# Performance work log

Measured on AMD Instinct MI355X. Metric: run time of the kernel, lower is better.

Reference implementation:

```python
import jax, jax.numpy as jnp
import numpy as np
from jax import lax

N = 200; E = 3200; HID = 64; NH = 16; OUT = 2 * HID; CAT = NH * OUT  # CAT = 2048
ALPHA = 0.2


def _gat(h, e_attr, adj, n2n, W, a_s, a_d, a_e, We, concat):
    # edge-feature-aware GAT head: logits from Wh_i, Wh_j and projected node2node feats
    Nn = h.shape[0]
    Wh = h @ W                                       # [N, out]
    ee = ((n2n @ We) @ a_e).reshape(Nn, Nn)          # [N, N] edge-feature term
    logits = jax.nn.leaky_relu((Wh @ a_s)[:, None] + (Wh @ a_d)[None, :] + ee,
                               negative_slope=ALPHA)
    logits = jnp.where(adj > 0, logits, -1e9)        # mask to graph structure
    att = jax.nn.softmax(logits, axis=1)
    h2 = att @ Wh
    if concat:
        h2 = jax.nn.elu(h2)
    return h2, jax.nn.elu(e_attr @ We)               # updated node + edge features


def _edge_pool(x, eidx, e, w, b):
    # static-shape edge pooling: score edges, gate nodes by mean incident score
    src, dst = eidx[0], eidx[1]
    s = jax.nn.sigmoid(jnp.concatenate([x[src], x[dst], e], axis=1) @ w + b)  # [E]
    deg = jax.ops.segment_sum(jnp.ones_like(s), src, num_segments=x.shape[0])
    ns = jax.ops.segment_sum(s, src, num_segments=x.shape[0]) / (deg + 1e-6)
    return x * ns[:, None], e * s[:, None]


def _gpool(x, w, b):
    # GlobalAttention: gate_nn = Linear+Sigmoid, softmax over nodes, weighted sum
    gate = jax.nn.softmax(jax.nn.sigmoid(x @ w + b), axis=0)  # [N, 1]
    return jnp.sum(gate * x, axis=0, keepdims=True)           # [1, D]


def _adj_n2n(Nn, eidx, eattr):
    # vectorized version of the per-edge Python loop in _get_adj_node2node
    src, dst = eidx[0], eidx[1]
    adj = jnp.zeros((Nn, Nn), eattr.dtype).at[src, dst].set(1.0)
    n2n = jnp.zeros((Nn * Nn, eattr.shape[1]), eattr.dtype).at[src * Nn + dst].set(eattr)
    return adj, n2n


def _lstm_dir(x, Wih, Whh, b):
    # one LSTM direction over seq x [T, Din] (PyTorch i,f,g,o gate order)
    Hh = Whh.shape[1]
    def step(carry, xt):
        h, c = carry
        g = xt @ Wih.T + h @ Whh.T + b
        i, f, gg, o = jnp.split(g, 4)
        c = jax.nn.sigmoid(f) * c + jax.nn.sigmoid(i) * jnp.tanh(gg)
        h = jax.nn.sigmoid(o) * jnp.tanh(c)
        return (h, c), h
    (_, _), ys = lax.scan(step, (jnp.zeros(Hh, x.dtype), jnp.zeros(Hh, x.dtype)), x)
    return ys


def setup_inputs():
    key = jax.random.key(0)
    ks = iter(jax.random.split(key, 64))
    def rn(shape, scale=0.05):
        return jax.random.normal(next(ks), shape, jnp.float32) * scale
    inp = {}
    for g in (1, 2):
        eidx = jax.random.randint(next(ks), (2, E), 0, N)
        eattr = rn((E, HID), 1.0)
        adj, n2n = _adj_n2n(N, eidx, eattr)
        inp['features%d' % g] = rn((N, HID), 1.0)
        inp['edge_index%d' % g] = eidx
        inp['edgesAttr%d' % g] = eattr
        inp['adjacency%d' % g] = adj
        inp['node2node%d' % g] = n2n
    inp.update(dict(
        W_h=rn((HID, HID)),
        W_gat=rn((NH, HID, OUT)), a_src=rn((NH, OUT)), a_dst=rn((NH, OUT)),
        a_e=rn((NH, OUT)), We_gat=rn((NH, HID, OUT)),
        W_out=rn((CAT, OUT)), ao_src=rn((OUT,)), ao_dst=rn((OUT,)), ao_e=rn((OUT,)),
        We_out=rn((CAT, OUT)),
        ep1_w=rn((3 * CAT,)), ep1_b=rn(()),
        ep2_w=rn((3 * OUT,)), ep2_b=rn(()),
        g1_w=rn((HID, 1)), g1_b=rn((1,)),
        g2_w=rn((CAT, 1)), g2_b=rn((1,)),
        g3_w=rn((OUT, 1)), g3_b=rn((1,)),
        Wih0=rn((2, 512, 35 * HID)), Whh0=rn((2, 512, 128)), b0=rn((2, 512)),
        Wih1=rn((2, 512, 256)), Whh1=rn((2, 512, 128)), b1=rn((2, 512)),
        fc_w=rn((256, 2)), fc_b=rn((2,)),
    ))
    return inp


def reference(features1, features2, edge_index1, edge_index2, edgesAttr1, edgesAttr2,
              adjacency1, adjacency2, node2node1, node2node2,
              W_h, W_gat, a_src, a_dst, a_e, We_gat,
              W_out, ao_src, ao_dst, ao_e, We_out,
              ep1_w, ep1_b, ep2_w, ep2_b,
              g1_w, g1_b, g2_w, g2_b, g3_w, g3_b,
              Wih0, Whh0, b0, Wih1, Whh1, b1, fc_w, fc_b):
    def graph(feat, eidx, eattr, adj, n2n):
        h = jax.nn.elu(feat @ W_h)                              # SingleNodeAttentionLayer
        hs = [_gpool(h, g1_w, g1_b)]
        outs = [_gat(h, eattr, adj, n2n, W_gat[i], a_src[i], a_dst[i], a_e[i],
                     We_gat[i], True) for i in range(NH)]
        h = jnp.concatenate([o[0] for o in outs], axis=1)       # [N, 2048]
        eattr = jnp.concatenate([o[1] for o in outs], axis=1)   # [E, 2048]
        h, eattr = _edge_pool(h, eidx, eattr, ep1_w, ep1_b)
        hs.append(_gpool(h, g2_w, g2_b))
        adj2, n2n2 = _adj_n2n(h.shape[0], eidx, eattr)          # dense [N*N, 2048]
        h, eattr = _gat(h, eattr, adj2, n2n2, W_out, ao_src, ao_dst, ao_e, We_out, False)
        h, eattr = _edge_pool(h, eidx, eattr, ep2_w, ep2_b)
        hs.append(_gpool(h, g3_w, g3_b))
        return jnp.concatenate(hs, axis=1)                      # [1, 35*HID]

    h1 = graph(features1, edge_index1, edgesAttr1, adjacency1, node2node1)
    h2 = graph(features2, edge_index2, edgesAttr2, adjacency2, node2node2)
    x = jnp.concatenate([h1, h2], axis=0)                       # seq [2, 2240]
    for Wih, Whh, b in ((Wih0, Whh0, b0), (Wih1, Whh1, b1)):
        f = _lstm_dir(x, Wih[0], Whh[0], b[0])
        r = _lstm_dir(x[::-1], Wih[1], Whh[1], b[1])[::-1]
        x = jnp.concatenate([f, r], axis=1)                     # [2, 256]
    logits = x[-1] @ fc_w + fc_b
    return jax.nn.softmax(logits)[None, :]                      # [1, nclass]
```

## Files before the change

kernel.cpp:

```cpp
#include <hip/hip_runtime.h>
#include <math.h>

#define DI static __device__ __forceinline__

DI float eluf(float x){ return x > 0.f ? x : expm1f(x); }
DI float lreluf(float x){ return x > 0.f ? x : 0.2f*x; }
DI float sigmf(float x){ return 1.f/(1.f+expf(-x)); }

typedef unsigned short u16;
typedef unsigned int   u32;
typedef __attribute__((ext_vector_type(8))) short short8_t;
typedef __attribute__((ext_vector_type(4))) float f32x4;

DI u16 bf16rne(float f){
  u32 u = __float_as_uint(f);
  u += 0x7fffu + ((u>>16)&1u);
  return (u16)(u>>16);
}

DI f32x4 bmfma(short8_t a, short8_t b, f32x4 c){
  return __builtin_amdgcn_mfma_f32_16x16x32_bf16(a, b, c, 0, 0, 0);
}

constexpr int N=200, E=3200, HID=64, NH=16, OUTD=128, CAT=2048, SEQD=2240;

constexpr int OH0   = 0;
constexpr int OWH   = OH0 + N*HID;
constexpr int OASN  = OWH + NH*N*OUTD;
constexpr int OADN  = OASN + NH*N;
constexpr int OH1   = OADN + NH*N;
constexpr int OXW1  = OH1 + N*CAT;
constexpr int OXW2  = OXW1 + 256;
constexpr int OEW1  = OXW2 + 256;
constexpr int OS1   = OEW1 + E;
constexpr int ODEG1 = OS1 + E;
constexpr int OSS1  = ODEG1 + 256;
constexpr int ORAW1 = OSS1 + 256;
constexpr int OWH2  = ORAW1 + 256;
constexpr int OAS2  = OWH2 + N*OUTD;
constexpr int OAD2  = OAS2 + 256;
constexpr int OEWV  = OAD2 + 256;
constexpr int OH2B  = OEWV + E;
constexpr int OXS2  = OH2B + N*OUTD;
constexpr int OXD2  = OXS2 + 256;
constexpr int ODEG2 = OXD2 + 256;
constexpr int OSS2  = ODEG2 + 256;
constexpr int ORAW2 = OSS2 + 256;
constexpr int ORAW3 = ORAW2 + 256;
constexpr int PGF   = ORAW3 + 256;
constexpr int GLOBF = 10624;
constexpr int TOTF  = GLOBF + 2*PGF;

__device__ __attribute__((aligned(16))) float G_F[TOTF];
__device__ float G_E2PART[(size_t)4*2*E*OUTD];
__device__ float G_EDOTH[2*NH*E];
__device__ float G_WHHT[2*2*128*512];
__device__ int   G_PIDX[2*N*N];
__device__ __attribute__((aligned(16))) u16 G_WGAT_T[NH*OUTD*HID];
__device__ __attribute__((aligned(16))) u16 G_WOUT_T[OUTD*CAT];
__device__ __attribute__((aligned(16))) u16 G_EATTR_BF[2*E*HID];

DI float* gf(int g){ return G_F + GLOBF + (size_t)g*PGF; }
DI float* gwe_ae(){ return G_F; }
DI float* gv_e(){ return G_F + 1024; }
DI float* gy0(){ return G_F + 3072; }
DI float* gy1(){ return G_F + 3584; }
DI float* gxseq(){ return G_F + 4096; }
DI float* gxg(){ return G_F + 8576; }
DI int*   gpidx(int g){ return G_PIDX + g*N*N; }

struct GraphIn {
  const float *feat, *eattr, *adj, *n2n;
  const int   *eidx;
};

struct Params {
  GraphIn g[2];
  const float *W_h, *W_gat, *a_src, *a_dst, *a_e, *We_gat;
  const float *W_out, *ao_src, *ao_dst, *ao_e, *We_out;
  const float *ep1_w, *ep1_b, *ep2_w, *ep2_b;
  const float *g1_w, *g1_b, *g2_w, *g2_b, *g3_w, *g3_b;
  const float *Wih0, *Whh0, *b0, *Wih1, *Whh1, *b1, *fc_w, *fc_b;
  float *out;
};

constexpr int ZPG  = 2*E + 1024;
constexpr int IB_Z = (2*ZPG+255)/256;
constexpr int IB_C = (2*N*N+255)/256;
constexpr int IB_D = 32;
constexpr int IB_E = (NH*HID+CAT+3)/4;
constexpr int IB_H = (2*N+3)/4;
constexpr int IB_W1 = 16;
constexpr int IB_W2 = 32;
constexpr int IB_EA = (2*E*HID)/256;
constexpr int IB_TOT = IB_Z+IB_C+IB_D+IB_E+IB_H+IB_W1+IB_W2+IB_EA;
__global__ __launch_bounds__(256) void k_init(Params P){
  __shared__ __attribute__((aligned(16))) float ldt[8320];
  int b = blockIdx.x, tid = threadIdx.x;
  if (b < IB_Z){
    int i = b*256 + tid;
    if (i < 2*ZPG){
      int g = i/ZPG, r = i%ZPG;
      int addr = r<E ? OEW1+r : (r<2*E ? OEWV+(r-E) :
                 (r<2*E+512 ? ODEG1+(r-2*E) : ODEG2+(r-2*E-512)));
      gf(g)[addr] = 0.f;
    }
  } else if (b < IB_Z+IB_C){
    int i = (b-IB_Z)*256 + tid; if (i < 2*N*N) G_PIDX[i] = -1;
  } else if (b < IB_Z+IB_C+IB_D){
    int tt = b-(IB_Z+IB_C);
    int ld = tt>>3, gt0 = (tt&7)*64;
    int l = ld>>1, d = ld&1;
    const float* Whh = l ? P.Whh1 : P.Whh0;
    const float* src = Whh + ((size_t)d*512 + gt0)*128;
    #pragma unroll
    for (int i=0;i<32;i++){
      int idx = tid + i*256;
      int gl = idx>>7, k = idx&127;
      ldt[gl*129 + k] = src[idx];
    }
    __syncthreads();
    float* dst = G_WHHT + (size_t)ld*128*512 + gt0;
    #pragma unroll
    for (int i=0;i<32;i++){
      int idx = tid + i*256;
      int gl = idx&63, k = idx>>6;
      dst[(size_t)k*512 + gl] = ldt[gl*129 + k];
    }
  } else if (b < IB_Z+IB_C+IB_D+IB_E){
    int gid = (b-IB_Z-IB_C-IB_D)*4 + (tid>>6);
    int lane = tid & 63;
    if (gid < NH*HID){
      int h = gid/HID, c = gid%HID;
      const float* W = P.We_gat + (size_t)(h*HID+c)*OUTD;
      const float* a = P.a_e + h*OUTD;
      float acc = 0.f;
      for (int o=lane;o<OUTD;o+=64) acc += W[o]*a[o];
      for (int off=32;off>0;off>>=1) acc += __shfl_down(acc,off);
      if (lane==0) gwe_ae()[gid] = acc;
    } else if (gid < NH*HID+CAT){
      int c = gid - NH*HID;
      const float* W = P.We_out + (size_t)c*OUTD;
      float acc = 0.f;
      for (int o=lane;o<OUTD;o+=64) acc += W[o]*P.ao_e[o];
      for (int off=32;off>0;off>>=1) acc += __shfl_down(acc,off);
      if (lane==0) gv_e()[c] = acc;
    }
  } else if (b < IB_Z+IB_C+IB_D+IB_E+IB_H){
    int unit = (b-IB_Z-IB_C-IB_D-IB_E)*4 + (tid>>6);
    if (unit >= 2*N) return;
    int g = unit / N, n = unit % N, c = tid & 63;
    const float* feat = P.g[g].feat;
    float acc = 0.f;
    for (int k=0;k<HID;k++) acc += feat[n*HID+k]*P.W_h[k*HID+c];
    float v = eluf(acc);
    float* f = gf(g);
    f[OH0 + n*HID + c] = v;
    float r = v*P.g1_w[c];
    for (int off=32;off>0;off>>=1) r += __shfl_down(r,off);
    if (c==0) f[ORAW1+n] = r;
  } else if (b < IB_Z+IB_C+IB_D+IB_E+IB_H+IB_W1){
    int h = b-(IB_Z+IB_C+IB_D+IB_E+IB_H);
    const float* src = P.We_gat + (size_t)h*HID*OUTD;
    #pragma unroll
    for (int i=0;i<32;i++){
      int idx = tid + i*256;
      int c = idx>>7, o = idx&127;
      ldt[o*65 + c] = src[idx];
    }
    __syncthreads();
    u16* dst = G_WGAT_T + (size_t)h*OUTD*HID;
    #pragma unroll
    for (int i=0;i<32;i++){
      int idx = tid + i*256;
      int c = idx&63, o = idx>>6;
      dst[o*64 + c] = bf16rne(ldt[o*65 + c]);
    }
  } else if (b < IB_Z+IB_C+IB_D+IB_E+IB_H+IB_W1+IB_W2){
    int tt = b-(IB_Z+IB_C+IB_D+IB_E+IB_H+IB_W1);
    int q0 = (tt>>1)*128, n0 = (tt&1)*64;
    #pragma unroll
    for (int i=0;i<32;i++){
      int idx = tid + i*256;
      int nl = idx&63, ql = idx>>6;
      ldt[ql*65 + nl] = P.We_out[(size_t)(q0+ql)*OUTD + n0 + nl];
    }
    __syncthreads();
    #pragma unroll
    for (int i=0;i<32;i++){
      int idx = tid + i*256;
      int ql = idx&127, nl = idx>>7;
      G_WOUT_T[(size_t)(n0+nl)*CAT + q0 + ql] = bf16rne(ldt[ql*65 + nl]);
    }
  } else {
    int i = (b-(IB_Z+IB_C+IB_D+IB_E+IB_H+IB_W1+IB_W2))*256 + tid;
    int g = i >= E*HID ? 1 : 0;
    G_EATTR_BF[i] = bf16rne(P.g[g].eattr[i - g*E*HID]);
  }
}


DI void e2p_body(Params& P, int idx, char* smem){
  int g = idx/400, r2 = idx%400, hg = r2/100, eb = r2%100;
  int tid = threadIdx.x;
  int wave = tid>>6, lane = tid&63, l16 = lane&15, l4 = lane>>4;
  u16* Tlds = (u16*)smem;
  int e0 = eb*32;
  int nt0 = wave*2;
  const u16* ea = G_EATTR_BF + ((size_t)g*E + e0)*HID;
  short8_t af00 = *(const short8_t*)(ea + l16*HID + l4*8);
  short8_t af01 = *(const short8_t*)(ea + l16*HID + 32 + l4*8);
  short8_t af10 = *(const short8_t*)(ea + (16+l16)*HID + l4*8);
  short8_t af11 = *(const short8_t*)(ea + (16+l16)*HID + 32 + l4*8);
  float ew1p0[4] = {0.f,0.f,0.f,0.f}, ewvp0[4] = {0.f,0.f,0.f,0.f};
  float ew1p1[4] = {0.f,0.f,0.f,0.f}, ewvp1[4] = {0.f,0.f,0.f,0.f};
  for (int hh=0; hh<4; hh++){
    int h = hg*4 + hh;
    const u16* Wg = G_WGAT_T + (size_t)h*OUTD*HID;
    #pragma unroll
    for (int nn=0; nn<2; nn++){
      int nt = nt0 + nn;
      const u16* Wgn = Wg + (size_t)(nt*16 + l16)*HID + l4*8;
      short8_t wg0 = *(const short8_t*)Wgn;
      short8_t wg1 = *(const short8_t*)(Wgn + 32);
      f32x4 d0 = {0.f,0.f,0.f,0.f}, d1 = {0.f,0.f,0.f,0.f};
      d0 = bmfma(af00, wg0, d0);
      d1 = bmfma(af10, wg0, d1);
      d0 = bmfma(af01, wg1, d0);
      d1 = bmfma(af11, wg1, d1);
      int qg = h*OUTD + nt*16 + l16;
      float w1 = P.ep1_w[2*CAT + qg];
      float wv = gv_e()[qg];
      int qloc = hh*128 + nt*16 + l16;
      #pragma unroll
      for (int r=0;r<4;r++){
        float v0 = d0[r] > 0.f ? d0[r] : expm1f(d0[r]);
        float v1 = d1[r] > 0.f ? d1[r] : expm1f(d1[r]);
        ew1p0[r] += v0*w1; ewvp0[r] += v0*wv;
        ew1p1[r] += v1*w1; ewvp1[r] += v1*wv;
        int row = l4*4 + r;
        int byt = (row*1024 + qloc*2) ^ ((row&7)<<4);
        *(u16*)((char*)Tlds + byt) = bf16rne(v0);
        *(u16*)((char*)Tlds + byt + 16384) = bf16rne(v1);
      }
    }
  }
  const u16* WoA = G_WOUT_T + (size_t)(wave*32 + l16)*CAT + hg*512 + l4*8;
  const u16* WoB = WoA + 16*CAT;
  short8_t w0a = *(const short8_t*)WoA;
  short8_t w0b = *(const short8_t*)WoB;
  short8_t w1a = *(const short8_t*)(WoA + 32);
  short8_t w1b = *(const short8_t*)(WoB + 32);
  float* f = gf(g);
  #pragma unroll
  for (int r=0;r<4;r++){
    float a0 = ew1p0[r], b0 = ewvp0[r], a1 = ew1p1[r], b1 = ewvp1[r];
    a0 += __shfl_xor(a0,1); b0 += __shfl_xor(b0,1); a1 += __shfl_xor(a1,1); b1 += __shfl_xor(b1,1);
    a0 += __shfl_xor(a0,2); b0 += __shfl_xor(b0,2); a1 += __shfl_xor(a1,2); b1 += __shfl_xor(b1,2);
    a0 += __shfl_xor(a0,4); b0 += __shfl_xor(b0,4); a1 += __shfl_xor(a1,4); b1 += __shfl_xor(b1,4);
    a0 += __shfl_xor(a0,8); b0 += __shfl_xor(b0,8); a1 += __shfl_xor(a1,8); b1 += __shfl_xor(b1,8);
    if (l16==0){
      int e = e0 + l4*4 + r;
      atomicAdd(&f[OEW1+e], a0);
      atomicAdd(&f[OEWV+e], b0);
      atomicAdd(&f[OEW1+e+16], a1);
      atomicAdd(&f[OEWV+e+16], b1);
    }
  }
  __syncthreads();
  f32x4 acc00 = {0.f,0.f,0.f,0.f}, acc01 = {0.f,0.f,0.f,0.f};
  f32x4 acc10 = {0.f,0.f,0.f,0.f}, acc11 = {0.f,0.f,0.f,0.f};
  #pragma unroll
  for (int ks=0; ks<16; ks++){
    short8_t na = w0a, nb = w0b;
    if (ks < 14){
      na = *(const short8_t*)(WoA + (ks+2)*32);
      nb = *(const short8_t*)(WoB + (ks+2)*32);
    }
    int byt = (l16*1024 + ks*64 + l4*16) ^ ((l16&7)<<4);
    short8_t a0 = *(const short8_t*)((const char*)Tlds + byt);
    short8_t a1 = *(const short8_t*)((const char*)Tlds + byt + 16384);
    acc00 = bmfma(a0, w0a, acc00);
    acc10 = bmfma(a1, w0a, acc10);
    acc01 = bmfma(a0, w0b, acc01);
    acc11 = bmfma(a1, w0b, acc11);
    w0a = w1a; w0b = w1b; w1a = na; w1b = nb;
  }
  float* dst = G_E2PART + (((size_t)hg*2 + g)*E + e0)*OUTD;
  #pragma unroll
  for (int r=0;r<4;r++){
    int ee = l4*4 + r;
    dst[(size_t)ee*OUTD + wave*32 + l16]      = acc00[r];
    dst[(size_t)ee*OUTD + wave*32 + 16 + l16] = acc01[r];
    dst[(size_t)(16+ee)*OUTD + wave*32 + l16]      = acc10[r];
    dst[(size_t)(16+ee)*OUTD + wave*32 + 16 + l16] = acc11[r];
  }
}

DI void edoth_body(Params& P, int idx, float* s){
  int tid = threadIdx.x;
  int g = idx / (E/16);
  int e0 = (idx % (E/16)) * 16;
  float (*ea)[HID+1] = (float(*)[HID+1])s;
  float (*wa)[HID+1] = (float(*)[HID+1])(s + 16*(HID+1));
  {
    int row = tid >> 4, c0 = (tid & 15)*4;
    float4 v = *(const float4*)&P.g[g].eattr[(size_t)(e0+row)*HID + c0];
    ea[row][c0]=v.x; ea[row][c0+1]=v.y; ea[row][c0+2]=v.z; ea[row][c0+3]=v.w;
    float4 w = *(const float4*)&gwe_ae()[row*HID + c0];
    wa[row][c0]=w.x; wa[row][c0+1]=w.y; wa[row][c0+2]=w.z; wa[row][c0+3]=w.w;
  }
  __syncthreads();
  int h = tid >> 4, el = tid & 15;
  float acc = 0.f;
  #pragma unroll
  for (int c=0;c<HID;c++) acc += ea[el][c]*wa[h][c];
  G_EDOTH[((size_t)g*NH + h)*E + e0 + el] = acc;
}

DI void wh_body(Params& P, int idx, float* s){
  int o = threadIdx.x;
  if (o >= 128) return;
  int g = idx / (N*(NH+1));
  int r = idx % (N*(NH+1));
  int h = r / N, n = r % N;
  float* f = gf(g);
  if (h == NH){
    if (n != 0) return;
    float* att = s;
    float* sb  = s + 200;
    for (int j = o; j < N; j += 128) att[j] = sigmf(f[ORAW1+j] + P.g1_b[0]);
    __syncthreads();
    float m = -3e38f;
    for (int j = o; j < N; j += 128) m = fmaxf(m, att[j]);
    sb[o] = m; __syncthreads();
    for (int sft=64;sft>0;sft>>=1){ if (o<sft) sb[o]=fmaxf(sb[o],sb[o+sft]); __syncthreads(); }
    m = sb[0]; __syncthreads();
    float ss = 0.f;
    for (int j = o; j < N; j += 128){ float e = expf(att[j]-m); ss += e; }
    sb[o] = ss; __syncthreads();
    for (int sft=64;sft>0;sft>>=1){ if (o<sft) sb[o]+=sb[o+sft]; __syncthreads(); }
    float inv = 1.f/sb[0]; __syncthreads();
    for (int j = o; j < N; j += 128) att[j] = expf(att[j]-m)*inv;
    __syncthreads();
    if (o < HID){
      float acc = 0.f;
      for (int j=0;j<N;j++) acc += att[j]*f[OH0 + j*HID + o];
      gxseq()[g*SEQD + o] = acc;
    }
    return;
  }
  float* hs   = s;
  float* sred = s + 64;
  float* dred = s + 192;
  if (o < HID) hs[o] = f[OH0 + n*HID + o];
  __syncthreads();
  const float* W = P.W_gat + (size_t)h*HID*OUTD + o;
  float acc = 0.f;
  for (int c=0;c<HID;c++) acc += hs[c]*W[(size_t)c*OUTD];
  f[OWH + ((size_t)h*N + n)*OUTD + o] = acc;
  sred[o] = acc*P.a_src[h*OUTD+o];
  dred[o] = acc*P.a_dst[h*OUTD+o];
  __syncthreads();
  for (int sft=64;sft>0;sft>>=1){ if (o<sft){ sred[o]+=sred[o+sft]; dred[o]+=dred[o+sft]; } __syncthreads(); }
  if (o==0){ f[OASN+h*N+n]=sred[0]; f[OADN+h*N+n]=dred[0]; }
}

DI void pairs_body(Params& P, int idx){
  int g = idx / 13;
  int e = (idx % 13)*256 + threadIdx.x;
  if (e >= E) return;
  const int* ei = P.g[g].eidx;
  atomicMax(&gpidx(g)[ei[e]*N + ei[E+e]], e);
}

DI void att1_body(Params& P, int idx, float* s){
  int tid = threadIdx.x;
  if (tid >= 128) return;
  int g = idx / 800;
  int r2 = idx % 800;
  int h = r2 / 50, nb = r2 % 50;
  int n0 = nb*4;
  float (*z)[N] = (float(*)[N])s;
  float* red  = s + 800;
  float* sinv = s + 928;
  float* f = gf(g);
  const float* adj = P.g[g].adj;
  const int* pidx = gpidx(g);
  const float* edoth = G_EDOTH + ((size_t)g*NH + h)*E;
  const float* adn = f + OADN + h*N;
  for (int i=0;i<4;i++){
    float asn = f[OASN + h*N + n0+i];
    for (int j = tid; j < N; j += 128){
      float a = adj[(n0+i)*N + j];
      float zz;
      if (a > 0.f){
        int p = pidx[(n0+i)*N + j];
        float ee = (p >= 0) ? edoth[p] : 0.f;
        zz = lreluf(asn + adn[j] + ee);
      } else zz = -1e9f;
      z[i][j] = zz;
    }
  }
  __syncthreads();
  for (int i=0;i<4;i++){
    float m = -3e38f;
    for (int j = tid; j < N; j += 128) m = fmaxf(m, z[i][j]);
    red[tid] = m; __syncthreads();
    for (int ss=64;ss>0;ss>>=1){ if (tid<ss) red[tid]=fmaxf(red[tid],red[tid+ss]); __syncthreads(); }
    m = red[0]; __syncthreads();
    float ssum = 0.f;
    for (int j = tid; j < N; j += 128){ float e = expf(z[i][j]-m); z[i][j]=e; ssum += e; }
    red[tid] = ssum; __syncthreads();
    for (int ss=64;ss>0;ss>>=1){ if (tid<ss) red[tid]+=red[tid+ss]; __syncthreads(); }
    if (tid==0) sinv[i] = 1.f/red[0];
    __syncthreads();
  }
  const float* wh = f + OWH + (size_t)h*N*OUTD;
  float a0=0.f,a1=0.f,a2=0.f,a3=0.f;
  for (int j=0;j<N;j++){
    float w = wh[(size_t)j*OUTD + tid];
    a0 += z[0][j]*w; a1 += z[1][j]*w; a2 += z[2][j]*w; a3 += z[3][j]*w;
  }
  f[OH1 + (size_t)(n0+0)*CAT + h*OUTD + tid] = eluf(a0*sinv[0]);
  f[OH1 + (size_t)(n0+1)*CAT + h*OUTD + tid] = eluf(a1*sinv[1]);
  f[OH1 + (size_t)(n0+2)*CAT + h*OUTD + tid] = eluf(a2*sinv[2]);
  f[OH1 + (size_t)(n0+3)*CAT + h*OUTD + tid] = eluf(a3*sinv[3]);
}

constexpr int MA_ED = 400, MA_WH = 2*N*(NH+1), MA_PR = 26;
__global__ __launch_bounds__(256) void k_mega_a(Params P){
  __shared__ __attribute__((aligned(16))) float smem[2080];
  int b = blockIdx.x;
  if (b < MA_ED) edoth_body(P, b, smem);
  else if (b < MA_ED+MA_WH) wh_body(P, b-MA_ED, smem);
  else pairs_body(P, b-(MA_ED+MA_WH));
}

constexpr int MB_E2P = 800, MB_A1 = 1600;
__global__ __launch_bounds__(256) void k_mega_b(Params P){
  __shared__ __attribute__((aligned(16))) char smem[32768];
  int b = blockIdx.x;
  if (b < MB_E2P) e2p_body(P, b, smem);
  else att1_body(P, b-MB_E2P, (float*)smem);
}

__global__ void k_xw1(Params P){
  int n = blockIdx.x, g = blockIdx.y, tid = threadIdx.x;
  __shared__ float s1b[256], s2b[256], s3b[256];
  float* f = gf(g);
  const float* x = f + OH1 + (size_t)n*CAT;
  float a1 = 0.f, a2 = 0.f, a3 = 0.f;
  for (int c = tid; c < CAT; c += 256){
    float xv = x[c];
    a1 += xv*P.ep1_w[c];
    a2 += xv*P.ep1_w[CAT+c];
    a3 += xv*P.g2_w[c];
  }
  s1b[tid]=a1; s2b[tid]=a2; s3b[tid]=a3; __syncthreads();
  for (int s=128;s>0;s>>=1){
    if (tid<s){ s1b[tid]+=s1b[tid+s]; s2b[tid]+=s2b[tid+s]; s3b[tid]+=s3b[tid+s]; }
    __syncthreads();
  }
  if (tid==0){ f[OXW1+n]=s1b[0]; f[OXW2+n]=s2b[0]; f[ORAW2+n]=s3b[0]; }
}

__global__ void k_s1(Params P){
  int e = blockIdx.x*256 + threadIdx.x, g = blockIdx.y;
  if (e >= E) return;
  float* f = gf(g);
  const int* ei = P.g[g].eidx;
  int s = ei[e], d = ei[E+e];
  float v = sigmf(f[OXW1+s] + f[OXW2+d] + f[OEW1+e] + P.ep1_b[0]);
  f[OS1+e] = v;
  atomicAdd(&f[OSS1+s], v);
  atomicAdd(&f[ODEG1+s], 1.f);
}

DI void gpool_body(Params& P, int xoff, int D, int odeg, int rawoff,
                   const float* bb, int outoff, int cb, int g,
                   float* att, float* sb){
  int tid = threadIdx.x;
  float* f = gf(g);
  if (tid < N){
    float sc = f[odeg+256+tid]/(f[odeg+tid]+1e-6f);
    att[tid] = sigmf(f[rawoff+tid]*sc + bb[0]);
  }
  __syncthreads();
  float m = (tid < N) ? att[tid] : -3e38f;
  sb[tid] = m; __syncthreads();
  for (int s=256;s>0;s>>=1){ if (tid<s) sb[tid]=fmaxf(sb[tid],sb[tid+s]); __syncthreads(); }
  m = sb[0]; __syncthreads();
  float e = (tid < N) ? expf(att[tid]-m) : 0.f;
  sb[tid] = e; __syncthreads();
  for (int s=256;s>0;s>>=1){ if (tid<s) sb[tid]+=sb[tid+s]; __syncthreads(); }
  float inv = 1.f/sb[0]; __syncthreads();
  if (tid < N){
    float sc = f[odeg+256+tid]/(f[odeg+tid]+1e-6f);
    att[tid] = e*inv*sc;
  }
  __syncthreads();
  int c = cb*512 + tid;
  if (c < D){
    const float* x = f + xoff;
    float acc = 0.f;
    for (int n=0;n<N;n++) acc += att[n]*x[(size_t)n*D + c];
    gxseq()[g*SEQD + outoff + c] = acc;
  }
}

DI void wh2_body(Params& P, int n, int g, float* hrow4, float* part4,
                 float* sr, float* dr){
  int tid = threadIdx.x;
  int kq = tid >> 7, o = tid & 127;
  float (*hrow)[128] = (float(*)[128])hrow4;
  float (*part)[128] = (float(*)[128])part4;
  float* f = gf(g);
  const float* x = f + OH1 + (size_t)n*CAT;
  float acc = 0.f;
  for (int cc=0; cc<4; cc++){
    int c0 = kq*512 + cc*128;
    __syncthreads();
    hrow[kq][o] = x[c0 + o];
    __syncthreads();
    const float* W = P.W_out + (size_t)c0*OUTD + o;
    for (int j=0;j<128;j++) acc += hrow[kq][j]*W[(size_t)j*OUTD];
  }
  part[kq][o] = acc;
  __syncthreads();
  if (kq==0){
    float ns = f[OSS1+n]/(f[ODEG1+n]+1e-6f);
    float a = part[0][o]+part[1][o]+part[2][o]+part[3][o];
    float v = a*ns;
    f[OWH2 + (size_t)n*OUTD + o] = v;
    sr[o] = v*P.ao_src[o];
    dr[o] = v*P.ao_dst[o];
  }
  __syncthreads();
  for (int s=64;s>0;s>>=1){
    if (tid<s){ sr[tid]+=sr[tid+s]; dr[tid]+=dr[tid+s]; }
    __syncthreads();
  }
  if (tid==0){ f[OAS2+n]=sr[0]; f[OAD2+n]=dr[0]; }
}

__global__ __launch_bounds__(512) void k_wh2p2(Params P){
  __shared__ float sa[512], sbb[512], sc2[128], sd[128];
  int b = blockIdx.x;
  if (b < 400){
    wh2_body(P, b>>1, b&1, sa, sbb, sc2, sd);
  } else {
    int idx = b-400, g = idx>>2, cb = idx&3;
    gpool_body(P, OH1, CAT, ODEG1, ORAW2, P.g2_b, HID, cb, g, sa, sbb);
  }
}

__global__ __launch_bounds__(512) void k_pool3(Params P){
  __shared__ float att[256];
  __shared__ float sb[512];
  int g = blockIdx.x;
  gpool_body(P, OH2B, OUTD, ODEG2, ORAW3, P.g3_b, HID+CAT, 0, g, att, sb);
}

__global__ void k_att2(Params P){
  int n = blockIdx.x, g = blockIdx.y, tid = threadIdx.x;
  __shared__ float z[N];
  __shared__ float red[128];
  __shared__ float dred[128];
  __shared__ float gred[128];
  float* f = gf(g);
  const float* adj = P.g[g].adj;
  const int* pidx = gpidx(g);
  float asn = f[OAS2+n];
  const float* adn = f + OAD2;
  for (int j = tid; j < N; j += 128){
    float a = adj[n*N + j];
    float zz;
    if (a > 0.f){
      int p = pidx[n*N + j];
      float ee = (p >= 0) ? f[OEWV+p]*f[OS1+p] : 0.f;
      zz = lreluf(asn + adn[j] + ee);
    } else zz = -1e9f;
    z[j] = zz;
  }
  __syncthreads();
  float m = -3e38f;
  for (int j = tid; j < N; j += 128) m = fmaxf(m, z[j]);
  red[tid] = m; __syncthreads();
  for (int s=64;s>0;s>>=1){ if (tid<s) red[tid]=fmaxf(red[tid],red[tid+s]); __syncthreads(); }
  m = red[0]; __syncthreads();
  float ssum = 0.f;
  for (int j = tid; j < N; j += 128){ float e = expf(z[j]-m); z[j]=e; ssum += e; }
  red[tid] = ssum; __syncthreads();
  for (int s=64;s>0;s>>=1){ if (tid<s) red[tid]+=red[tid+s]; __syncthreads(); }
  float inv = 1.f/red[0]; __syncthreads();
  const float* wh = f + OWH2;
  float acc = 0.f;
  for (int j=0;j<N;j++){
    float w = z[j];
    if (w != 0.f) acc += w * wh[(size_t)j*OUTD + tid];
  }
  float v = acc*inv;
  f[OH2B + (size_t)n*OUTD + tid] = v;
  red[tid]  = v*P.ep2_w[tid];
  dred[tid] = v*P.ep2_w[OUTD+tid];
  gred[tid] = v*P.g3_w[tid];
  __syncthreads();
  for (int s=64;s>0;s>>=1){
    if (tid<s){ red[tid]+=red[tid+s]; dred[tid]+=dred[tid+s]; gred[tid]+=gred[tid+s]; }
    __syncthreads();
  }
  if (tid==0){ f[OXS2+n]=red[0]; f[OXD2+n]=dred[0]; f[ORAW3+n]=gred[0]; }
}

constexpr int TE2 = 16;
__global__ void k_ew2fin(Params P){
  int e0 = blockIdx.x*TE2, g = blockIdx.y, tid = threadIdx.x;
  __shared__ float lred[2][TE2];
  float* f = gf(g);
  float w2 = P.ep2_w[2*OUTD + tid];
  int lane = tid & 63, wvi = tid >> 6;
  for (int e=0;e<TE2;e++){
    const float* src = G_E2PART + ((size_t)g*E + e0 + e)*OUTD + tid;
    float a = 0.f;
    #pragma unroll
    for (int h=0;h<4;h++) a += src[(size_t)h*2*E*OUTD];
    float v = eluf(f[OS1+e0+e]*a) * w2;
    for (int off=32;off>0;off>>=1) v += __shfl_down(v,off);
    if (lane==0) lred[wvi][e]=v;
  }
  __syncthreads();
  if (tid < TE2){
    int e = e0 + tid;
    float ew2 = lred[0][tid]+lred[1][tid];
    const int* ei = P.g[g].eidx;
    int s = ei[e], d = ei[E+e];
    float v = sigmf(f[OXS2+s] + f[OXD2+d] + ew2 + P.ep2_b[0]);
    atomicAdd(&f[OSS2+s], v);
    atomicAdd(&f[ODEG2+s], 1.f);
  }
}

__global__ void k_lstm_xg(Params P, int layer){
  int gid = blockIdx.x*4 + (threadIdx.x>>6);
  int lane = threadIdx.x & 63;
  int t = gid >> 10;
  int rem = gid & 1023;
  int d = rem >> 9;
  int gate = rem & 511;
  const float* Wih = layer ? P.Wih1 : P.Wih0;
  const float* bb  = layer ? P.b1   : P.b0;
  const float* xin = layer ? gy0()  : gxseq();
  int Din = layer ? 256 : SEQD;
  const float* x = xin + t*Din;
  const float* Wr = Wih + ((size_t)d*512 + gate)*Din;
  float acc = 0.f;
  for (int k=lane; k<Din; k+=64) acc += x[k]*Wr[k];
  for (int off=32; off>0; off>>=1) acc += __shfl_down(acc, off);
  if (lane==0) gxg()[(t*2 + d)*512 + gate] = acc + bb[d*512 + gate];
}

__global__ void k_lstm_rec(Params P, int layer){
  int d = blockIdx.x, tid = threadIdx.x;
  float* yout = layer ? gy1() : gy0();
  const float* T = G_WHHT + (size_t)(layer*2 + d)*128*512;
  __shared__ float h[128], c[128], gbuf[512];
  if (tid < 128){ h[tid]=0.f; c[tid]=0.f; }
  __syncthreads();
  for (int s=0;s<2;s++){
    int t = (d==0) ? s : 1-s;
    float acc = gxg()[(t*2 + d)*512 + tid];
    for (int k=0;k<128;k++) acc += h[k]*T[(size_t)k*512 + tid];
    gbuf[tid] = acc;
    __syncthreads();
    if (tid < 128){
      float ii = sigmf(gbuf[tid]);
      float ff = sigmf(gbuf[128+tid]);
      float gg = tanhf(gbuf[256+tid]);
      float oo = sigmf(gbuf[384+tid]);
      float cn = ff*c[tid] + ii*gg;
      c[tid] = cn;
      float hn = oo*tanhf(cn);
      h[tid] = hn;
      yout[t*256 + d*128 + tid] = hn;
    }
    __syncthreads();
  }
}

__global__ __launch_bounds__(1024) void k_recfin(Params P){
  int tid = threadIdx.x;
  int d = tid>>9, gt = tid&511;
  __shared__ float h[2][128], c[2][128], gbuf[2][512], yfin[256];
  __shared__ float sb[256], sb2[256];
  if (gt < 128){ h[d][gt]=0.f; c[d][gt]=0.f; }
  __syncthreads();
  const float* T = G_WHHT + (size_t)(2 + d)*128*512;
  for (int s=0;s<2;s++){
    int t = (d==0) ? s : 1-s;
    float acc = gxg()[(t*2 + d)*512 + gt];
    for (int k=0;k<128;k++) acc += h[d][k]*T[(size_t)k*512 + gt];
    gbuf[d][gt] = acc;
    __syncthreads();
    if (gt < 128){
      float ii = sigmf(gbuf[d][gt]);
      float ff = sigmf(gbuf[d][128+gt]);
      float gg = tanhf(gbuf[d][256+gt]);
      float oo = sigmf(gbuf[d][384+gt]);
      float cn = ff*c[d][gt] + ii*gg;
      c[d][gt] = cn;
      float hn = oo*tanhf(cn);
      h[d][gt] = hn;
      if (t==1) yfin[d*128 + gt] = hn;
    }
    __syncthreads();
  }
  if (tid < 256){
    sb[tid]  = yfin[tid]*P.fc_w[tid*2+0];
    sb2[tid] = yfin[tid]*P.fc_w[tid*2+1];
  }
  __syncthreads();
  for (int s=128;s>0;s>>=1){
    if (tid<s){ sb[tid]+=sb[tid+s]; sb2[tid]+=sb2[tid+s]; }
    __syncthreads();
  }
  if (tid==0){
    float l0 = sb[0] + P.fc_b[0];
    float l1 = sb2[0] + P.fc_b[1];
    float m = fmaxf(l0,l1);
    float e0 = expf(l0-m), e1 = expf(l1-m), inv = 1.f/(e0+e1);
    P.out[0] = e0*inv;
    P.out[1] = e1*inv;
  }
}

extern "C" void kernel_launch(void* const* d_in, const int* in_sizes, int n_in,
                              void* d_out, int out_size, void* d_ws, size_t ws_size,
                              hipStream_t stream){
  Params P;
  for (int g=0; g<2; ++g){
    int b = g*5;
    P.g[g].feat  = (const float*)d_in[b+0];
    P.g[g].eidx  = (const int*)d_in[b+1];
    P.g[g].eattr = (const float*)d_in[b+2];
    P.g[g].adj   = (const float*)d_in[b+3];
    P.g[g].n2n   = (const float*)d_in[b+4];
  }
  P.W_h   = (const float*)d_in[10];
  P.W_gat = (const float*)d_in[11];
  P.a_src = (const float*)d_in[12];
  P.a_dst = (const float*)d_in[13];
  P.a_e   = (const float*)d_in[14];
  P.We_gat= (const float*)d_in[15];
  P.W_out = (const float*)d_in[16];
  P.ao_src= (const float*)d_in[17];
  P.ao_dst= (const float*)d_in[18];
  P.ao_e  = (const float*)d_in[19];
  P.We_out= (const float*)d_in[20];
  P.ep1_w = (const float*)d_in[21];
  P.ep1_b = (const float*)d_in[22];
  P.ep2_w = (const float*)d_in[23];
  P.ep2_b = (const float*)d_in[24];
  P.g1_w  = (const float*)d_in[25];
  P.g1_b  = (const float*)d_in[26];
  P.g2_w  = (const float*)d_in[27];
  P.g2_b  = (const float*)d_in[28];
  P.g3_w  = (const float*)d_in[29];
  P.g3_b  = (const float*)d_in[30];
  P.Wih0  = (const float*)d_in[31];
  P.Whh0  = (const float*)d_in[32];
  P.b0    = (const float*)d_in[33];
  P.Wih1  = (const float*)d_in[34];
  P.Whh1  = (const float*)d_in[35];
  P.b1    = (const float*)d_in[36];
  P.fc_w  = (const float*)d_in[37];
  P.fc_b  = (const float*)d_in[38];
  P.out   = (float*)d_out;

  k_init  <<<dim3(IB_TOT), 256, 0, stream>>>(P);
  k_mega_a<<<dim3(MA_ED+MA_WH+MA_PR), 256, 0, stream>>>(P);
  k_mega_b<<<dim3(MB_E2P+MB_A1), 256, 0, stream>>>(P);
  k_xw1   <<<dim3(N,2),    256, 0, stream>>>(P);
  k_s1    <<<dim3((E+255)/256,2), 256, 0, stream>>>(P);
  k_wh2p2 <<<dim3(408),    512, 0, stream>>>(P);
  k_att2  <<<dim3(N,2),    128, 0, stream>>>(P);
  k_ew2fin<<<dim3(E/TE2,2),128, 0, stream>>>(P);
  k_pool3 <<<dim3(2),      512, 0, stream>>>(P);
  k_lstm_xg <<<dim3(512),  256, 0, stream>>>(P, 0);
  k_lstm_rec<<<dim3(2),    512, 0, stream>>>(P, 0);
  k_lstm_xg <<<dim3(512),  256, 0, stream>>>(P, 1);
  k_recfin<<<dim3(1),     1024, 0, stream>>>(P);
}
```

Before: 351.3 us.

## Fuse tail stages into one cooperative persistent kernel with grid syncs

Replaces ten small tail kernel launches (xw1, s1, wh2/pool2, att2, ew2fin, pool3, LSTM input projections and recurrences, final fc) with a single cooperative kernel of 256 blocks that steps through the stages separated by grid.sync. It also overlaps pool3 with most of the layer-0 LSTM input projection by splitting the 2240-wide dot product into a gxseq-independent part and a remainder. k_mega_b now interleaves its e2p and att1 blocks by block index. The aim is to remove per-launch overhead and idle gaps between tiny dependent kernels, at the cost of grid-wide barrier latency and fixed-size blocks that underuse threads in some stages.

Result: slower. 643.0 us (+83.1%).

```diff
diff --git a/kernel.cpp b/kernel.cpp
--- a/kernel.cpp
+++ b/kernel.cpp
@@ -1,5 +1,8 @@
 #include <hip/hip_runtime.h>
+#include <hip/hip_cooperative_groups.h>
 #include <math.h>
+
+namespace cg = cooperative_groups;
 
 #define DI static __device__ __forceinline__
 
@@ -437,44 +440,13 @@
   else pairs_body(P, b-(MA_ED+MA_WH));
 }
 
-constexpr int MB_E2P = 800, MB_A1 = 1600;
+constexpr int MB_TOT = 2400;
 __global__ __launch_bounds__(256) void k_mega_b(Params P){
   __shared__ __attribute__((aligned(16))) char smem[32768];
   int b = blockIdx.x;
-  if (b < MB_E2P) e2p_body(P, b, smem);
-  else att1_body(P, b-MB_E2P, (float*)smem);
-}
-
-__global__ void k_xw1(Params P){
-  int n = blockIdx.x, g = blockIdx.y, tid = threadIdx.x;
-  __shared__ float s1b[256], s2b[256], s3b[256];
-  float* f = gf(g);
-  const float* x = f + OH1 + (size_t)n*CAT;
-  float a1 = 0.f, a2 = 0.f, a3 = 0.f;
-  for (int c = tid; c < CAT; c += 256){
-    float xv = x[c];
-    a1 += xv*P.ep1_w[c];
-    a2 += xv*P.ep1_w[CAT+c];
-    a3 += xv*P.g2_w[c];
-  }
-  s1b[tid]=a1; s2b[tid]=a2; s3b[tid]=a3; __syncthreads();
-  for (int s=128;s>0;s>>=1){
-    if (tid<s){ s1b[tid]+=s1b[tid+s]; s2b[tid]+=s2b[tid+s]; s3b[tid]+=s3b[tid+s]; }
-    __syncthreads();
-  }
-  if (tid==0){ f[OXW1+n]=s1b[0]; f[OXW2+n]=s2b[0]; f[ORAW2+n]=s3b[0]; }
-}
-
-__global__ void k_s1(Params P){
-  int e = blockIdx.x*256 + threadIdx.x, g = blockIdx.y;
-  if (e >= E) return;
-  float* f = gf(g);
-  const int* ei = P.g[g].eidx;
-  int s = ei[e], d = ei[E+e];
-  float v = sigmf(f[OXW1+s] + f[OXW2+d] + f[OEW1+e] + P.ep1_b[0]);
-  f[OS1+e] = v;
-  atomicAdd(&f[OSS1+s], v);
-  atomicAdd(&f[ODEG1+s], 1.f);
+  int r = b % 3, vb = b / 3;
+  if (r == 0) e2p_body(P, vb, smem);
+  else att1_body(P, vb*2 + (r-1), (float*)smem);
 }
 
 DI void gpool_body(Params& P, int xoff, int D, int odeg, int rawoff,
@@ -507,6 +479,7 @@
     for (int n=0;n<N;n++) acc += att[n]*x[(size_t)n*D + c];
     gxseq()[g*SEQD + outoff + c] = acc;
   }
+  __syncthreads();
 }
 
 DI void wh2_body(Params& P, int n, int g, float* hrow4, float* part4,
@@ -542,195 +515,274 @@
     __syncthreads();
   }
   if (tid==0){ f[OAS2+n]=sr[0]; f[OAD2+n]=dr[0]; }
-}
-
-__global__ __launch_bounds__(512) void k_wh2p2(Params P){
-  __shared__ float sa[512], sbb[512], sc2[128], sd[128];
-  int b = blockIdx.x;
-  if (b < 400){
-    wh2_body(P, b>>1, b&1, sa, sbb, sc2, sd);
-  } else {
-    int idx = b-400, g = idx>>2, cb = idx&3;
-    gpool_body(P, OH1, CAT, ODEG1, ORAW2, P.g2_b, HID, cb, g, sa, sbb);
-  }
-}
-
-__global__ __launch_bounds__(512) void k_pool3(Params P){
-  __shared__ float att[256];
-  __shared__ float sb[512];
-  int g = blockIdx.x;
-  gpool_body(P, OH2B, OUTD, ODEG2, ORAW3, P.g3_b, HID+CAT, 0, g, att, sb);
-}
-
-__global__ void k_att2(Params P){
-  int n = blockIdx.x, g = blockIdx.y, tid = threadIdx.x;
-  __shared__ float z[N];
-  __shared__ float red[128];
-  __shared__ float dred[128];
-  __shared__ float gred[128];
-  float* f = gf(g);
-  const float* adj = P.g[g].adj;
-  const int* pidx = gpidx(g);
-  float asn = f[OAS2+n];
-  const float* adn = f + OAD2;
-  for (int j = tid; j < N; j += 128){
-    float a = adj[n*N + j];
-    float zz;
-    if (a > 0.f){
-      int p = pidx[n*N + j];
-      float ee = (p >= 0) ? f[OEWV+p]*f[OS1+p] : 0.f;
-      zz = lreluf(asn + adn[j] + ee);
-    } else zz = -1e9f;
-    z[j] = zz;
-  }
-  __syncthreads();
-  float m = -3e38f;
-  for (int j = tid; j < N; j += 128) m = fmaxf(m, z[j]);
-  red[tid] = m; __syncthreads();
-  for (int s=64;s>0;s>>=1){ if (tid<s) red[tid]=fmaxf(red[tid],red[tid+s]); __syncthreads(); }
-  m = red[0]; __syncthreads();
-  float ssum = 0.f;
-  for (int j = tid; j < N; j += 128){ float e = expf(z[j]-m); z[j]=e; ssum += e; }
-  red[tid] = ssum; __syncthreads();
-  for (int s=64;s>0;s>>=1){ if (tid<s) red[tid]+=red[tid+s]; __syncthreads(); }
-  float inv = 1.f/red[0]; __syncthreads();
-  const float* wh = f + OWH2;
-  float acc = 0.f;
-  for (int j=0;j<N;j++){
-    float w = z[j];
-    if (w != 0.f) acc += w * wh[(size_t)j*OUTD + tid];
-  }
-  float v = acc*inv;
-  f[OH2B + (size_t)n*OUTD + tid] = v;
-  red[tid]  = v*P.ep2_w[tid];
-  dred[tid] = v*P.ep2_w[OUTD+tid];
-  gred[tid] = v*P.g3_w[tid];
-  __syncthreads();
-  for (int s=64;s>0;s>>=1){
-    if (tid<s){ red[tid]+=red[tid+s]; dred[tid]+=dred[tid+s]; gred[tid]+=gred[tid+s]; }
-    __syncthreads();
-  }
-  if (tid==0){ f[OXS2+n]=red[0]; f[OXD2+n]=dred[0]; f[ORAW3+n]=gred[0]; }
-}
-
+  __syncthreads();
+}
+
+constexpr int CG_GRID = 256;
 constexpr int TE2 = 16;
-__global__ void k_ew2fin(Params P){
-  int e0 = blockIdx.x*TE2, g = blockIdx.y, tid = threadIdx.x;
-  __shared__ float lred[2][TE2];
-  float* f = gf(g);
-  float w2 = P.ep2_w[2*OUTD + tid];
-  int lane = tid & 63, wvi = tid >> 6;
-  for (int e=0;e<TE2;e++){
-    const float* src = G_E2PART + ((size_t)g*E + e0 + e)*OUTD + tid;
-    float a = 0.f;
-    #pragma unroll
-    for (int h=0;h<4;h++) a += src[(size_t)h*2*E*OUTD];
-    float v = eluf(f[OS1+e0+e]*a) * w2;
-    for (int off=32;off>0;off>>=1) v += __shfl_down(v,off);
-    if (lane==0) lred[wvi][e]=v;
-  }
-  __syncthreads();
-  if (tid < TE2){
-    int e = e0 + tid;
-    float ew2 = lred[0][tid]+lred[1][tid];
-    const int* ei = P.g[g].eidx;
-    int s = ei[e], d = ei[E+e];
-    float v = sigmf(f[OXS2+s] + f[OXD2+d] + ew2 + P.ep2_b[0]);
-    atomicAdd(&f[OSS2+s], v);
-    atomicAdd(&f[ODEG2+s], 1.f);
-  }
-}
-
-__global__ void k_lstm_xg(Params P, int layer){
-  int gid = blockIdx.x*4 + (threadIdx.x>>6);
-  int lane = threadIdx.x & 63;
-  int t = gid >> 10;
-  int rem = gid & 1023;
-  int d = rem >> 9;
-  int gate = rem & 511;
-  const float* Wih = layer ? P.Wih1 : P.Wih0;
-  const float* bb  = layer ? P.b1   : P.b0;
-  const float* xin = layer ? gy0()  : gxseq();
-  int Din = layer ? 256 : SEQD;
-  const float* x = xin + t*Din;
-  const float* Wr = Wih + ((size_t)d*512 + gate)*Din;
-  float acc = 0.f;
-  for (int k=lane; k<Din; k+=64) acc += x[k]*Wr[k];
-  for (int off=32; off>0; off>>=1) acc += __shfl_down(acc, off);
-  if (lane==0) gxg()[(t*2 + d)*512 + gate] = acc + bb[d*512 + gate];
-}
-
-__global__ void k_lstm_rec(Params P, int layer){
-  int d = blockIdx.x, tid = threadIdx.x;
-  float* yout = layer ? gy1() : gy0();
-  const float* T = G_WHHT + (size_t)(layer*2 + d)*128*512;
-  __shared__ float h[128], c[128], gbuf[512];
-  if (tid < 128){ h[tid]=0.f; c[tid]=0.f; }
-  __syncthreads();
-  for (int s=0;s<2;s++){
-    int t = (d==0) ? s : 1-s;
-    float acc = gxg()[(t*2 + d)*512 + tid];
-    for (int k=0;k<128;k++) acc += h[k]*T[(size_t)k*512 + tid];
-    gbuf[tid] = acc;
-    __syncthreads();
-    if (tid < 128){
-      float ii = sigmf(gbuf[tid]);
-      float ff = sigmf(gbuf[128+tid]);
-      float gg = tanhf(gbuf[256+tid]);
-      float oo = sigmf(gbuf[384+tid]);
-      float cn = ff*c[tid] + ii*gg;
-      c[tid] = cn;
-      float hn = oo*tanhf(cn);
-      h[tid] = hn;
-      yout[t*256 + d*128 + tid] = hn;
-    }
-    __syncthreads();
-  }
-}
-
-__global__ __launch_bounds__(1024) void k_recfin(Params P){
+__global__ __launch_bounds__(512) void k_tail(Params P){
+  cg::grid_group grid = cg::this_grid();
   int tid = threadIdx.x;
-  int d = tid>>9, gt = tid&511;
-  __shared__ float h[2][128], c[2][128], gbuf[2][512], yfin[256];
-  __shared__ float sb[256], sb2[256];
-  if (gt < 128){ h[d][gt]=0.f; c[d][gt]=0.f; }
-  __syncthreads();
-  const float* T = G_WHHT + (size_t)(2 + d)*128*512;
-  for (int s=0;s<2;s++){
-    int t = (d==0) ? s : 1-s;
-    float acc = gxg()[(t*2 + d)*512 + gt];
-    for (int k=0;k<128;k++) acc += h[d][k]*T[(size_t)k*512 + gt];
-    gbuf[d][gt] = acc;
-    __syncthreads();
-    if (gt < 128){
-      float ii = sigmf(gbuf[d][gt]);
-      float ff = sigmf(gbuf[d][128+gt]);
-      float gg = tanhf(gbuf[d][256+gt]);
-      float oo = sigmf(gbuf[d][384+gt]);
-      float cn = ff*c[d][gt] + ii*gg;
-      c[d][gt] = cn;
-      float hn = oo*tanhf(cn);
-      h[d][gt] = hn;
-      if (t==1) yfin[d*128 + gt] = hn;
-    }
-    __syncthreads();
-  }
-  if (tid < 256){
-    sb[tid]  = yfin[tid]*P.fc_w[tid*2+0];
-    sb2[tid] = yfin[tid]*P.fc_w[tid*2+1];
-  }
-  __syncthreads();
-  for (int s=128;s>0;s>>=1){
-    if (tid<s){ sb[tid]+=sb[tid+s]; sb2[tid]+=sb2[tid+s]; }
-    __syncthreads();
-  }
-  if (tid==0){
-    float l0 = sb[0] + P.fc_b[0];
-    float l1 = sb2[0] + P.fc_b[1];
-    float m = fmaxf(l0,l1);
-    float e0 = expf(l0-m), e1 = expf(l1-m), inv = 1.f/(e0+e1);
-    P.out[0] = e0*inv;
-    P.out[1] = e1*inv;
+  __shared__ float smem[1600];
+
+  for (int vb = blockIdx.x; vb < 400; vb += CG_GRID){
+    int n = vb>>1, g = vb&1;
+    float* f = gf(g);
+    const float* x = f + OH1 + (size_t)n*CAT;
+    float a1 = 0.f, a2 = 0.f, a3 = 0.f;
+    for (int c = tid; c < CAT; c += 512){
+      float xv = x[c];
+      a1 += xv*P.ep1_w[c];
+      a2 += xv*P.ep1_w[CAT+c];
+      a3 += xv*P.g2_w[c];
+    }
+    float* s1b = smem; float* s2b = smem+512; float* s3b = smem+1024;
+    s1b[tid]=a1; s2b[tid]=a2; s3b[tid]=a3; __syncthreads();
+    for (int s=256;s>0;s>>=1){
+      if (tid<s){ s1b[tid]+=s1b[tid+s]; s2b[tid]+=s2b[tid+s]; s3b[tid]+=s3b[tid+s]; }
+      __syncthreads();
+    }
+    if (tid==0){ f[OXW1+n]=s1b[0]; f[OXW2+n]=s2b[0]; f[ORAW2+n]=s3b[0]; }
+    __syncthreads();
+  }
+  grid.sync();
+
+  for (int vb = blockIdx.x; vb < 14; vb += CG_GRID){
+    int g = vb/7;
+    int e = (vb%7)*512 + tid;
+    if (e < E){
+      float* f = gf(g);
+      const int* ei = P.g[g].eidx;
+      int s = ei[e], d = ei[E+e];
+      float v = sigmf(f[OXW1+s] + f[OXW2+d] + f[OEW1+e] + P.ep1_b[0]);
+      f[OS1+e] = v;
+      atomicAdd(&f[OSS1+s], v);
+      atomicAdd(&f[ODEG1+s], 1.f);
+    }
+  }
+  grid.sync();
+
+  for (int vb = blockIdx.x; vb < 408; vb += CG_GRID){
+    if (vb < 400) wh2_body(P, vb>>1, vb&1, smem, smem+512, smem+1024, smem+1152);
+    else {
+      int idx = vb-400, g = idx>>2, cb = idx&3;
+      gpool_body(P, OH1, CAT, ODEG1, ORAW2, P.g2_b, HID, cb, g, smem, smem+256);
+    }
+  }
+  grid.sync();
+
+  for (int vb = blockIdx.x; vb < 400; vb += CG_GRID){
+    int n = vb>>1, g = vb&1;
+    bool act = tid < 128;
+    float* z    = smem;
+    float* red  = smem+200;
+    float* dred = smem+328;
+    float* gred = smem+456;
+    float* f = gf(g);
+    const float* adj = P.g[g].adj;
+    const int* pidx = gpidx(g);
+    float asn = f[OAS2+n];
+    const float* adn = f + OAD2;
+    if (act){
+      for (int j = tid; j < N; j += 128){
+        float a = adj[n*N + j];
+        float zz;
+        if (a > 0.f){
+          int p = pidx[n*N + j];
+          float ee = (p >= 0) ? f[OEWV+p]*f[OS1+p] : 0.f;
+          zz = lreluf(asn + adn[j] + ee);
+        } else zz = -1e9f;
+        z[j] = zz;
+      }
+    }
+    __syncthreads();
+    float m = -3e38f;
+    if (act){ for (int j = tid; j < N; j += 128) m = fmaxf(m, z[j]); red[tid] = m; }
+    __syncthreads();
+    for (int s=64;s>0;s>>=1){ if (act && tid<s) red[tid]=fmaxf(red[tid],red[tid+s]); __syncthreads(); }
+    m = red[0]; __syncthreads();
+    float ssum = 0.f;
+    if (act){ for (int j = tid; j < N; j += 128){ float e = expf(z[j]-m); z[j]=e; ssum += e; } red[tid] = ssum; }
+    __syncthreads();
+    for (int s=64;s>0;s>>=1){ if (act && tid<s) red[tid]+=red[tid+s]; __syncthreads(); }
+    float inv = 1.f/red[0]; __syncthreads();
+    if (act){
+      const float* wh = f + OWH2;
+      float acc = 0.f;
+      for (int j=0;j<N;j++){
+        float w = z[j];
+        if (w != 0.f) acc += w * wh[(size_t)j*OUTD + tid];
+      }
+      float v = acc*inv;
+      f[OH2B + (size_t)n*OUTD + tid] = v;
+      red[tid]  = v*P.ep2_w[tid];
+      dred[tid] = v*P.ep2_w[OUTD+tid];
+      gred[tid] = v*P.g3_w[tid];
+    }
+    __syncthreads();
+    for (int s=64;s>0;s>>=1){
+      if (act && tid<s){ red[tid]+=red[tid+s]; dred[tid]+=dred[tid+s]; gred[tid]+=gred[tid+s]; }
+      __syncthreads();
+    }
+    if (tid==0){ f[OXS2+n]=red[0]; f[OXD2+n]=dred[0]; f[ORAW3+n]=gred[0]; }
+    __syncthreads();
+  }
+  grid.sync();
+
+  for (int vb = blockIdx.x; vb < 400; vb += CG_GRID){
+    int g = vb/200, eb = vb%200;
+    int e0 = eb*TE2;
+    bool act = tid < 128;
+    float* lred = smem;
+    float* f = gf(g);
+    if (act){
+      float w2 = P.ep2_w[2*OUTD + tid];
+      int lane = tid & 63, wvi = tid >> 6;
+      for (int e=0;e<TE2;e++){
+        const float* src = G_E2PART + ((size_t)g*E + e0 + e)*OUTD + tid;
+        float a = 0.f;
+        #pragma unroll
+        for (int h=0;h<4;h++) a += src[(size_t)h*2*E*OUTD];
+        float v = eluf(f[OS1+e0+e]*a) * w2;
+        for (int off=32;off>0;off>>=1) v += __shfl_down(v,off);
+        if (lane==0) lred[wvi*TE2+e]=v;
+      }
+    }
+    __syncthreads();
+    if (tid < TE2){
+      int e = e0 + tid;
+      float ew2 = lred[tid]+lred[TE2+tid];
+      const int* ei = P.g[g].eidx;
+      int s = ei[e], d = ei[E+e];
+      float v = sigmf(f[OXS2+s] + f[OXD2+d] + ew2 + P.ep2_b[0]);
+      atomicAdd(&f[OSS2+s], v);
+      atomicAdd(&f[ODEG2+s], 1.f);
+    }
+    __syncthreads();
+  }
+  grid.sync();
+
+  for (int vb = blockIdx.x; vb < 258; vb += CG_GRID){
+    if (vb < 2){
+      gpool_body(P, OH2B, OUTD, ODEG2, ORAW3, P.g3_b, HID+CAT, 0, vb, smem, smem+256);
+    } else {
+      int gid = (vb-2)*8 + (tid>>6);
+      int lane = tid & 63;
+      int t = gid >> 10, rem = gid & 1023, d = rem>>9, gate = rem&511;
+      const float* x = gxseq() + t*SEQD;
+      const float* Wr = P.Wih0 + ((size_t)d*512 + gate)*SEQD;
+      float acc = 0.f;
+      for (int k=lane; k<2112; k+=64) acc += x[k]*Wr[k];
+      for (int off=32; off>0; off>>=1) acc += __shfl_down(acc, off);
+      if (lane==0) gxg()[(t*2 + d)*512 + gate] = acc + P.b0[d*512 + gate];
+    }
+  }
+  grid.sync();
+
+  for (int vb = blockIdx.x; vb < 256; vb += CG_GRID){
+    int gid = vb*8 + (tid>>6);
+    int lane = tid & 63;
+    int t = gid >> 10, rem = gid & 1023, d = rem>>9, gate = rem&511;
+    const float* x = gxseq() + t*SEQD;
+    const float* Wr = P.Wih0 + ((size_t)d*512 + gate)*SEQD;
+    float acc = 0.f;
+    for (int k=2112+lane; k<SEQD; k+=64) acc += x[k]*Wr[k];
+    for (int off=32; off>0; off>>=1) acc += __shfl_down(acc, off);
+    if (lane==0) gxg()[(t*2 + d)*512 + gate] += acc;
+  }
+  grid.sync();
+
+  for (int vb = blockIdx.x; vb < 2; vb += CG_GRID){
+    int d = vb;
+    float* h = smem;
+    float* c = smem+128;
+    float* gbuf = smem+256;
+    const float* T = G_WHHT + (size_t)d*128*512;
+    if (tid < 128){ h[tid]=0.f; c[tid]=0.f; }
+    __syncthreads();
+    for (int s=0;s<2;s++){
+      int t = (d==0) ? s : 1-s;
+      float acc = gxg()[(t*2 + d)*512 + tid];
+      for (int k=0;k<128;k++) acc += h[k]*T[(size_t)k*512 + tid];
+      gbuf[tid] = acc;
+      __syncthreads();
+      if (tid < 128){
+        float ii = sigmf(gbuf[tid]);
+        float ff = sigmf(gbuf[128+tid]);
+        float gg = tanhf(gbuf[256+tid]);
+        float oo = sigmf(gbuf[384+tid]);
+        float cn = ff*c[tid] + ii*gg;
+        c[tid] = cn;
+        float hn = oo*tanhf(cn);
+        h[tid] = hn;
+        gy0()[t*256 + d*128 + tid] = hn;
+      }
+      __syncthreads();
+    }
+  }
+  grid.sync();
+
+  for (int vb = blockIdx.x; vb < 256; vb += CG_GRID){
+    int gid = vb*8 + (tid>>6);
+    int lane = tid & 63;
+    int t = gid >> 10, rem = gid & 1023, d = rem>>9, gate = rem&511;
+    const float* x = gy0() + t*256;
+    const float* Wr = P.Wih1 + ((size_t)d*512 + gate)*256;
+    float acc = 0.f;
+    for (int k=lane; k<256; k+=64) acc += x[k]*Wr[k];
+    for (int off=32; off>0; off>>=1) acc += __shfl_down(acc, off);
+    if (lane==0) gxg()[(t*2 + d)*512 + gate] = acc + P.b1[d*512 + gate];
+  }
+  grid.sync();
+
+  if (blockIdx.x == 0){
+    float* h    = smem;
+    float* c    = smem+128;
+    float* gbuf = smem+256;
+    float* yfin = smem+768;
+    float* sb   = smem+1024;
+    float* sb2  = smem+1280;
+    for (int d=0; d<2; ++d){
+      const float* T = G_WHHT + (size_t)(2 + d)*128*512;
+      if (tid < 128){ h[tid]=0.f; c[tid]=0.f; }
+      __syncthreads();
+      for (int s=0;s<2;s++){
+        int t = (d==0) ? s : 1-s;
+        float acc = gxg()[(t*2 + d)*512 + tid];
+        for (int k=0;k<128;k++) acc += h[k]*T[(size_t)k*512 + tid];
+        gbuf[tid] = acc;
+        __syncthreads();
+        if (tid < 128){
+          float ii = sigmf(gbuf[tid]);
+          float ff = sigmf(gbuf[128+tid]);
+          float gg = tanhf(gbuf[256+tid]);
+          float oo = sigmf(gbuf[384+tid]);
+          float cn = ff*c[tid] + ii*gg;
+          c[tid] = cn;
+          float hn = oo*tanhf(cn);
+          h[tid] = hn;
+          if (t==1) yfin[d*128 + tid] = hn;
+        }
+        __syncthreads();
+      }
+    }
+    if (tid < 256){
+      sb[tid]  = yfin[tid]*P.fc_w[tid*2+0];
+      sb2[tid] = yfin[tid]*P.fc_w[tid*2+1];
+    }
+    __syncthreads();
+    for (int s=128;s>0;s>>=1){
+      if (tid<s){ sb[tid]+=sb[tid+s]; sb2[tid]+=sb2[tid+s]; }
+      __syncthreads();
+    }
+    if (tid==0){
+      float l0 = sb[0] + P.fc_b[0];
+      float l1 = sb2[0] + P.fc_b[1];
+      float m = fmaxf(l0,l1);
+      float e0 = expf(l0-m), e1 = expf(l1-m), inv = 1.f/(e0+e1);
+      P.out[0] = e0*inv;
+      P.out[1] = e1*inv;
+    }
   }
 }
 
@@ -779,15 +831,7 @@
 
   k_init  <<<dim3(IB_TOT), 256, 0, stream>>>(P);
   k_mega_a<<<dim3(MA_ED+MA_WH+MA_PR), 256, 0, stream>>>(P);
-  k_mega_b<<<dim3(MB_E2P+MB_A1), 256, 0, stream>>>(P);
-  k_xw1   <<<dim3(N,2),    256, 0, stream>>>(P);
-  k_s1    <<<dim3((E+255)/256,2), 256, 0, stream>>>(P);
-  k_wh2p2 <<<dim3(408),    512, 0, stream>>>(P);
-  k_att2  <<<dim3(N,2),    128, 0, stream>>>(P);
-  k_ew2fin<<<dim3(E/TE2,2),128, 0, stream>>>(P);
-  k_pool3 <<<dim3(2),      512, 0, stream>>>(P);
-  k_lstm_xg <<<dim3(512),  256, 0, stream>>>(P, 0);
-  k_lstm_rec<<<dim3(2),    512, 0, stream>>>(P, 0);
-  k_lstm_xg <<<dim3(512),  256, 0, stream>>>(P, 1);
-  k_recfin<<<dim3(1),     1024, 0, stream>>>(P);
-}
+  k_mega_b<<<dim3(MB_TOT), 256, 0, stream>>>(P);
+  void* args[] = { (void*)&P };
+  hipLaunchCooperativeKernel((void*)k_tail, dim3(CG_GRID), dim3(512), args, 0, stream);
+}
```
